# Kernel tuning notes

Measured on AMD Instinct MI355X. Metric: run time of the kernel, lower is better.

## Reference

```python
import jax, jax.numpy as jnp
import numpy as np

TOP_K = 2
NUM_EXPERTS = 64
AUX_COEF = 0.01


def setup_inputs() -> dict:
    key = jax.random.key(0)
    kx, kw = jax.random.split(key)
    B, S, D, E = 4, 4096, 2048, NUM_EXPERTS
    x = jax.random.normal(kx, (B, S, D), dtype=jnp.float32)
    # nn.Linear default init ~ U(-1/sqrt(D), 1/sqrt(D))
    W = jax.random.uniform(kw, (E, D), dtype=jnp.float32,
                           minval=-1.0 / np.sqrt(D), maxval=1.0 / np.sqrt(D))
    return {"x": x, "W": W}


def reference(x, W):
    B, S, D = x.shape
    E = W.shape[0]
    # router projection (no bias)
    logits = jnp.einsum('bsd,ed->bse', x, W)          # [B,S,E]
    probs = jax.nn.softmax(logits, axis=-1)           # [B,S,E]
    top_k_gates, top_k_indices = jax.lax.top_k(probs, TOP_K)  # [B,S,K]
    top_k_gates = top_k_gates / (jnp.sum(top_k_gates, axis=-1, keepdims=True) + 1e-9)
    # aux loss: fraction of routed slots per expert (one-hot mean) x mean router prob
    total_slots = B * S * TOP_K
    counts = jnp.zeros((E,), dtype=jnp.float32).at[top_k_indices.reshape(-1)].add(1.0)
    avg_tokens_per_expert = counts / total_slots      # == one_hot(idx).mean(dims 0,1,2)
    avg_router_prob = jnp.mean(probs, axis=(0, 1))    # [E]
    aux_loss = AUX_COEF * E * jnp.sum(avg_tokens_per_expert * avg_router_prob)
    return top_k_indices, top_k_gates, aux_loss
```

## Files before the change

### kernel.cpp

```cpp
#include <hip/hip_runtime.h>
#include <math.h>

#define NTOK 16384
#define DDIM 2048
#define NEXP 64
#define TM   16
#define NBLK (NTOK / TM)
#define NCH  32
#define NS   64

typedef _Float16 half4v __attribute__((ext_vector_type(4)));
typedef _Float16 half8v __attribute__((ext_vector_type(8)));
typedef float    f32x4  __attribute__((ext_vector_type(4)));

#define MFMA16(a, b, c) __builtin_amdgcn_mfma_f32_16x16x32_f16((a), (b), (c), 0, 0, 0)

__global__ __launch_bounds__(256) void prep_kernel(const float* __restrict__ W,
                                                   _Float16* __restrict__ Wh,
                                                   _Float16* __restrict__ Wl,
                                                   float* __restrict__ accg) {
    int idx = blockIdx.x * 256 + threadIdx.x;
    int e = idx >> 11, k = idx & 2047;
    float w = W[idx];
    _Float16 h = (_Float16)w;
    _Float16 l = (_Float16)(w - (float)h);
    int S = k >> 5, nb = e >> 4, nl = e & 15, q = (k >> 3) & 3, j = k & 7;
    size_t off = (size_t)S * 2048 + nb * 512 + q * 128 + nl * 8 + j;
    Wh[off] = h;
    Wl[off] = l;
    if (blockIdx.x == 0 && threadIdx.x < 128) accg[threadIdx.x] = 0.0f;
}

__device__ inline void cvt_store(_Float16* __restrict__ Hp, _Float16* __restrict__ Lp,
                                 int off, float4 v) {
    half4v h, l;
    h.x = (_Float16)v.x; l.x = (_Float16)(v.x - (float)h.x);
    h.y = (_Float16)v.y; l.y = (_Float16)(v.y - (float)h.y);
    h.z = (_Float16)v.z; l.z = (_Float16)(v.z - (float)h.z);
    h.w = (_Float16)v.w; l.w = (_Float16)(v.w - (float)h.w);
    *(half4v*)&Hp[off] = h;
    *(half4v*)&Lp[off] = l;
}

__global__ __launch_bounds__(256) void router_kernel(
    const float* __restrict__ x, const _Float16* __restrict__ Wh,
    const _Float16* __restrict__ Wl, float* __restrict__ accg,
    float* __restrict__ out)
{
    __shared__ __align__(16) _Float16 Ah[2][1024];
    __shared__ __align__(16) _Float16 Al[2][1024];
    __shared__ float lgt[TM][NEXP + 1];
    __shared__ float cnt[NEXP];

    const int tid  = threadIdx.x;
    const int lane = tid & 63;
    const int wv   = __builtin_amdgcn_readfirstlane(tid >> 6);
    const int m0   = blockIdx.x * TM;

    if (tid < NEXP) cnt[tid] = 0.0f;

    const int tok0 = tid >> 4;
    const int kk0  = (tid & 15) * 4;
    const int s0   = kk0 >> 5, q0 = (kk0 >> 3) & 3, j00 = kk0 & 7;
    const int offA = (s0 * 64 + q0 * 16 + tok0) * 8 + j00;

    const float* gx = x + (size_t)(m0 + tok0) * DDIM + kk0;

    const _Float16* whp = Wh + wv * 512 + lane * 8;
    const _Float16* wlp = Wl + wv * 512 + lane * 8;

    f32x4 acc = {0.f, 0.f, 0.f, 0.f};

    float4 stg[2];
    stg[0] = *(const float4*)(gx);
    stg[1] = *(const float4*)(gx + 64);
    half8v wbh[2], wbl[2];
    #pragma unroll
    for (int s = 0; s < 2; ++s) {
        wbh[s] = *(const half8v*)(whp + (size_t)s * 2048);
        wbl[s] = *(const half8v*)(wlp + (size_t)s * 2048);
    }

    for (int ch = 0; ch < NCH; ++ch) {
        const int p = ch & 1;
        cvt_store(&Ah[p][0], &Al[p][0], offA, stg[p]);
        const int cf = (ch + 2 < NCH) ? ch + 2 : 0;
        stg[p] = *(const float4*)(gx + cf * 64);
        __syncthreads();
        #pragma unroll
        for (int s = 0; s < 2; ++s) {
            const int Sg  = ch * 2 + s;
            const int SgN = (Sg + 2) & (NS - 1);
            half8v ah = *(const half8v*)&Ah[p][(s * 64 + lane) * 8];
            half8v al = *(const half8v*)&Al[p][(s * 64 + lane) * 8];
            half8v bh = wbh[s], bl = wbl[s];
            wbh[s] = *(const half8v*)(whp + (size_t)SgN * 2048);
            wbl[s] = *(const half8v*)(wlp + (size_t)SgN * 2048);
            acc = MFMA16(al, bh, acc);
            acc = MFMA16(ah, bl, acc);
            acc = MFMA16(ah, bh, acc);
        }
    }

    {
        const int q  = lane >> 4;
        const int nl = lane & 15;
        #pragma unroll
        for (int r = 0; r < 4; ++r)
            lgt[q * 4 + r][wv * 16 + nl] = acc[r];
    }
    __syncthreads();

    if (tid < 128) {
        const int m = tid >> 3;
        const int j = tid & 7;
        float l[8];
        #pragma unroll
        for (int i = 0; i < 8; ++i) l[i] = lgt[m][j * 8 + i];

        float mx = l[0];
        #pragma unroll
        for (int i = 1; i < 8; ++i) mx = fmaxf(mx, l[i]);
        #pragma unroll
        for (int off = 1; off < 8; off <<= 1) mx = fmaxf(mx, __shfl_xor(mx, off, 8));

        float ev[8];
        float zs = 0.f;
        float v1 = -INFINITY, v2 = -INFINITY;
        int i1 = 0, i2 = 0;
        #pragma unroll
        for (int i = 0; i < 8; ++i) {
            ev[i] = __expf(l[i] - mx);
            zs += ev[i];
            int e = j * 8 + i;
            if (l[i] > v1)      { v2 = v1; i2 = i1; v1 = l[i]; i1 = e; }
            else if (l[i] > v2) { v2 = l[i]; i2 = e; }
        }
        #pragma unroll
        for (int off = 1; off < 8; off <<= 1) zs += __shfl_xor(zs, off, 8);

        #pragma unroll
        for (int off = 1; off < 8; off <<= 1) {
            float ov1 = __shfl_xor(v1, off, 8);
            int   oi1 = __shfl_xor(i1, off, 8);
            float ov2 = __shfl_xor(v2, off, 8);
            int   oi2 = __shfl_xor(i2, off, 8);
            bool afirst = (v1 > ov1) || (v1 == ov1 && i1 < oi1);
            if (afirst) {
                bool t = (v2 > ov1) || (v2 == ov1 && i2 < oi1);
                v2 = t ? v2 : ov1;
                i2 = t ? i2 : oi1;
            } else {
                bool t = (ov2 > v1) || (ov2 == v1 && oi2 < i1);
                v2 = t ? ov2 : v1;
                i2 = t ? oi2 : i1;
                v1 = ov1;
                i1 = oi1;
            }
        }

        const float invz = 1.0f / zs;
        if (j == 0) {
            float p1 = invz;
            float p2 = __expf(v2 - mx) * invz;
            float sden = p1 + p2 + 1e-9f;
            int tok = m0 + m;
            out[tok * 2 + 0] = (float)i1;
            out[tok * 2 + 1] = (float)i2;
            out[32768 + tok * 2 + 0] = p1 / sden;
            out[32768 + tok * 2 + 1] = p2 / sden;
            atomicAdd(&cnt[i1], 1.0f);
            atomicAdd(&cnt[i2], 1.0f);
        }

        #pragma unroll
        for (int i = 0; i < 8; ++i) lgt[m][j * 8 + i] = ev[i] * invz;
    }
    __syncthreads();

    if (tid < NEXP) {
        atomicAdd(&accg[tid], cnt[tid]);
    } else if (tid < 128) {
        int e = tid - 64;
        float s = 0.f;
        #pragma unroll
        for (int t = 0; t < TM; ++t) s += lgt[t][e];
        atomicAdd(&accg[64 + e], s);
    }
}

__global__ void finalize_kernel(const float* __restrict__ accg,
                                float* __restrict__ out)
{
    int t = threadIdx.x;
    float c = accg[t];
    float p = accg[64 + t];
    float term = (c / (float)(NTOK * 2)) * (p / (float)NTOK);
    #pragma unroll
    for (int off = 1; off < 64; off <<= 1) term += __shfl_xor(term, off, 64);
    if (t == 0) out[65536] = 0.01f * (float)NEXP * term;
}

extern "C" void kernel_launch(void* const* d_in, const int* in_sizes, int n_in,
                              void* d_out, int out_size, void* d_ws, size_t ws_size,
                              hipStream_t stream) {
    const float* x = (const float*)d_in[0];
    const float* W = (const float*)d_in[1];
    float* out  = (float*)d_out;
    float* accg = (float*)d_ws;
    _Float16* Wh = (_Float16*)(accg + 128);
    _Float16* Wl = Wh + (size_t)DDIM * NEXP;

    prep_kernel<<<512, 256, 0, stream>>>(W, Wh, Wl, accg);
    router_kernel<<<NBLK, 256, 0, stream>>>(x, Wh, Wl, accg, out);
    finalize_kernel<<<1, 64, 0, stream>>>(accg, out);
}
```

Baseline: 215.5 us.

## Deepen x prefetch to four chunks and use a raw LDS-only barrier

The router kernel now keeps four float4 chunks of x in flight per thread instead of two, to hide more global-load latency. The __syncthreads is replaced with an explicit lgkmcnt wait plus s_barrier, so the outstanding global loads are not drained at each chunk. Launch bounds request four waves per SIMD, and the weight prep kernel is vectorized to eight elements per thread with fewer blocks. The changes add register pressure and rely on the barrier only ordering LDS traffic being correct.

```diff
diff --git a/kernel.cpp b/kernel.cpp
--- a/kernel.cpp
+++ b/kernel.cpp
@@ -20,15 +20,25 @@
                                                    _Float16* __restrict__ Wl,
                                                    float* __restrict__ accg) {
     int idx = blockIdx.x * 256 + threadIdx.x;
-    int e = idx >> 11, k = idx & 2047;
-    float w = W[idx];
-    _Float16 h = (_Float16)w;
-    _Float16 l = (_Float16)(w - (float)h);
-    int S = k >> 5, nb = e >> 4, nl = e & 15, q = (k >> 3) & 3, j = k & 7;
-    size_t off = (size_t)S * 2048 + nb * 512 + q * 128 + nl * 8 + j;
-    Wh[off] = h;
-    Wl[off] = l;
-    if (blockIdx.x == 0 && threadIdx.x < 128) accg[threadIdx.x] = 0.0f;
+    int e  = idx >> 8;
+    int k0 = (idx & 255) << 3;
+    const float* wp = W + (size_t)e * DDIM + k0;
+    float4 w0 = *(const float4*)wp;
+    float4 w1 = *(const float4*)(wp + 4);
+    half8v h, l;
+    h[0] = (_Float16)w0.x; l[0] = (_Float16)(w0.x - (float)h[0]);
+    h[1] = (_Float16)w0.y; l[1] = (_Float16)(w0.y - (float)h[1]);
+    h[2] = (_Float16)w0.z; l[2] = (_Float16)(w0.z - (float)h[2]);
+    h[3] = (_Float16)w0.w; l[3] = (_Float16)(w0.w - (float)h[3]);
+    h[4] = (_Float16)w1.x; l[4] = (_Float16)(w1.x - (float)h[4]);
+    h[5] = (_Float16)w1.y; l[5] = (_Float16)(w1.y - (float)h[5]);
+    h[6] = (_Float16)w1.z; l[6] = (_Float16)(w1.z - (float)h[6]);
+    h[7] = (_Float16)w1.w; l[7] = (_Float16)(w1.w - (float)h[7]);
+    int S = k0 >> 5, nb = e >> 4, nl = e & 15, q = (k0 >> 3) & 3;
+    size_t off = (size_t)S * 2048 + nb * 512 + q * 128 + nl * 8;
+    *(half8v*)&Wh[off] = h;
+    *(half8v*)&Wl[off] = l;
+    if (idx < 128) accg[idx] = 0.0f;
 }
 
 __device__ inline void cvt_store(_Float16* __restrict__ Hp, _Float16* __restrict__ Lp,
@@ -42,7 +52,7 @@
     *(half4v*)&Lp[off] = l;
 }
 
-__global__ __launch_bounds__(256) void router_kernel(
+__global__ __launch_bounds__(256, 4) void router_kernel(
     const float* __restrict__ x, const _Float16* __restrict__ Wh,
     const _Float16* __restrict__ Wl, float* __restrict__ accg,
     float* __restrict__ out)
@@ -71,9 +81,9 @@
 
     f32x4 acc = {0.f, 0.f, 0.f, 0.f};
 
-    float4 stg[2];
-    stg[0] = *(const float4*)(gx);
-    stg[1] = *(const float4*)(gx + 64);
+    float4 stg[4];
+    #pragma unroll
+    for (int i = 0; i < 4; ++i) stg[i] = *(const float4*)(gx + i * 64);
     half8v wbh[2], wbl[2];
     #pragma unroll
     for (int s = 0; s < 2; ++s) {
@@ -83,10 +93,12 @@
 
     for (int ch = 0; ch < NCH; ++ch) {
         const int p = ch & 1;
-        cvt_store(&Ah[p][0], &Al[p][0], offA, stg[p]);
-        const int cf = (ch + 2 < NCH) ? ch + 2 : 0;
-        stg[p] = *(const float4*)(gx + cf * 64);
-        __syncthreads();
+        const int b = ch & 3;
+        cvt_store(&Ah[p][0], &Al[p][0], offA, stg[b]);
+        const int cf = (ch + 4 < NCH) ? ch + 4 : 0;
+        stg[b] = *(const float4*)(gx + cf * 64);
+        asm volatile("s_waitcnt lgkmcnt(0)" ::: "memory");
+        __builtin_amdgcn_s_barrier();
         #pragma unroll
         for (int s = 0; s < 2; ++s) {
             const int Sg  = ch * 2 + s;
@@ -211,7 +223,7 @@
     _Float16* Wh = (_Float16*)(accg + 128);
     _Float16* Wl = Wh + (size_t)DDIM * NEXP;
 
-    prep_kernel<<<512, 256, 0, stream>>>(W, Wh, Wl, accg);
+    prep_kernel<<<64, 256, 0, stream>>>(W, Wh, Wl, accg);
     router_kernel<<<NBLK, 256, 0, stream>>>(x, Wh, Wl, accg, out);
     finalize_kernel<<<1, 64, 0, stream>>>(accg, out);
 }
```

New measurement: 220.0 us. +2.1%, slower.
